# Performance work log

Measured on AMD Instinct MI355X. Metric: run time of the kernel, lower is better.

## Reference

```python
import jax, jax.numpy as jnp
import numpy as np

B, C = 8, 256
GRID = 128          # H = W = grid_size
N = GRID * GRID     # 16384 tokens
WS = 8              # swin window size
NH = 8              # num heads
DH = C // NH        # head dim = 32
HID = int(C * 4.0)  # mlp hidden = 1024
EPS = 1e-5


def _ln(x, g, b):
    m = jnp.mean(x, axis=-1, keepdims=True)
    v = jnp.mean(jnp.square(x - m), axis=-1, keepdims=True)
    return (x - m) * jax.lax.rsqrt(v + EPS) * g + b


def setup_inputs() -> dict:
    key = jax.random.key(0)
    ks = jax.random.split(key, 6)
    s = 0.02
    return {
        "x": jax.random.normal(ks[0], (B, N, C), jnp.float32),
        "ln1_g": jnp.ones((C,), jnp.float32), "ln1_b": jnp.zeros((C,), jnp.float32),
        "in_w": jax.random.normal(ks[1], (3 * C, C), jnp.float32) * s,
        "in_b": jnp.zeros((3 * C,), jnp.float32),
        "out_w": jax.random.normal(ks[2], (C, C), jnp.float32) * s,
        "out_b": jnp.zeros((C,), jnp.float32),
        "ln2_g": jnp.ones((C,), jnp.float32), "ln2_b": jnp.zeros((C,), jnp.float32),
        "w1": jax.random.normal(ks[3], (HID, C), jnp.float32) * s,
        "b1": jnp.zeros((HID,), jnp.float32),
        "w2": jax.random.normal(ks[4], (C, HID), jnp.float32) * s,
        "b2": jnp.zeros((C,), jnp.float32),
    }


def reference(x, ln1_g, ln1_b, in_w, in_b, out_w, out_b, ln2_g, ln2_b, w1, b1, w2, b2):
    shortcut = x
    xn = _ln(x, ln1_g, ln1_b)
    # window partition: [B,N,C] -> [B,H,W,C] -> [B*nW, WS*WS, C]
    xw = (xn.reshape(B, GRID // WS, WS, GRID // WS, WS, C)
            .transpose(0, 1, 3, 2, 4, 5)
            .reshape(-1, WS * WS, C))
    # torch nn.MultiheadAttention: fused in-proj, scale 1/sqrt(head_dim)
    qkv = xw @ in_w.T + in_b                      # [nW, T, 3C]
    q, k, v = jnp.split(qkv, 3, axis=-1)
    def heads(t):
        return t.reshape(t.shape[0], t.shape[1], NH, DH).transpose(0, 2, 1, 3)
    q, k, v = heads(q), heads(k), heads(v)        # [nW, NH, T, DH]
    scores = jnp.einsum('whtd,whsd->whts', q, k) * (1.0 / np.sqrt(DH))
    att = jax.nn.softmax(scores, axis=-1)
    o = jnp.einsum('whts,whsd->whtd', att, v)     # [nW, NH, T, DH]
    o = o.transpose(0, 2, 1, 3).reshape(-1, WS * WS, C)
    o = o @ out_w.T + out_b
    # window reverse: [B*nW, WS, WS, C] -> [B, N, C]
    x_attn = (o.reshape(B, GRID // WS, GRID // WS, WS, WS, C)
                .transpose(0, 1, 3, 2, 4, 5)
                .reshape(B, N, C))
    x = shortcut + x_attn
    h = _ln(x, ln2_g, ln2_b)
    h = jax.nn.gelu(h @ w1.T + b1, approximate=False)  # torch nn.GELU = exact erf
    return x + h @ w2.T + b2
```

## Files before the change

### kernel.cpp

```cpp
#include <hip/hip_runtime.h>
#include <hip/hip_bf16.h>
#include <cstdint>

#define DEVINL __device__ __forceinline__

using bf16 = __hip_bfloat16;
typedef __bf16 bf16x8 __attribute__((ext_vector_type(8)));
typedef float f32x4 __attribute__((ext_vector_type(4)));
typedef unsigned short u16x8 __attribute__((ext_vector_type(8)));

static constexpr int MTOK = 131072;

DEVINL void async_ld16(const void* g, void* l) {
  __builtin_amdgcn_global_load_lds(
      (__attribute__((address_space(1))) void*)(g),
      (__attribute__((address_space(3))) void*)(l), 16, 0, 0);
}

DEVINL unsigned short bfbits(float v) {
  bf16 h = __float2bfloat16(v);
  return *reinterpret_cast<unsigned short*>(&h);
}

DEVINL long pkaddr(long m, int k, int KP) {
  const long tile = m >> 7;
  const int row = (int)(m & 127);
  const int panel = k >> 6;
  const int c8 = ((k & 63) >> 3) ^ (row & 7);
  return ((tile * KP + panel) * 1024 + row * 8 + c8) * 8 + (k & 7);
}

__global__ __launch_bounds__(256) void cvt_w2(
    const float* __restrict__ ow, const float* __restrict__ w1,
    const float* __restrict__ w2, bf16* __restrict__ out) {
  int i = blockIdx.x * 256 + threadIdx.x;
  float v; long base; int n, k, KP;
  if (i < 65536)        { v = ow[i]; base = 0;      n = i >> 8;  k = i & 255;  KP = 4; }
  else if (i < 327680)  { int j = i - 65536;  v = w1[j]; base = 65536;  n = j >> 8;  k = j & 255;  KP = 4; }
  else                  { int j = i - 327680; v = w2[j]; base = 327680; n = j >> 10; k = j & 1023; KP = 16; }
  out[base + pkaddr(n, k, KP)] = __float2bfloat16(v);
}

template <bool REMAP>
__global__ __launch_bounds__(256) void ln_kern(
    const float* __restrict__ x, const float* __restrict__ gw,
    const float* __restrict__ bw, bf16* __restrict__ out) {
  const int lane = threadIdx.x & 63;
  const int wv = threadIdx.x >> 6;
  const long tok = (long)blockIdx.x * 4 + wv;
  const float4 v = *(const float4*)(x + tok * 256 + lane * 4);
  float s = v.x + v.y + v.z + v.w;
#pragma unroll
  for (int off = 32; off > 0; off >>= 1) s += __shfl_xor(s, off);
  const float mean = s * (1.0f / 256.0f);
  const float dx = v.x - mean, dy = v.y - mean, dz = v.z - mean, dw = v.w - mean;
  float q = dx * dx + dy * dy + dz * dz + dw * dw;
#pragma unroll
  for (int off = 32; off > 0; off >>= 1) q += __shfl_xor(q, off);
  const float inv = rsqrtf(q * (1.0f / 256.0f) + 1e-5f);
  long m;
  if (REMAP) {
    const int b = (int)(tok >> 14);
    const int n = (int)(tok & 16383);
    const int row = n >> 7, col = n & 127;
    const int w = b * 256 + (row >> 3) * 16 + (col >> 3);
    const int t = (row & 7) * 8 + (col & 7);
    m = (long)w * 64 + t;
  } else {
    m = tok;
  }
  const float4 g = *(const float4*)(gw + lane * 4);
  const float4 bb = *(const float4*)(bw + lane * 4);
  ushort4 o;
  o.x = bfbits(dx * inv * g.x + bb.x);
  o.y = bfbits(dy * inv * g.y + bb.y);
  o.z = bfbits(dz * inv * g.z + bb.z);
  o.w = bfbits(dw * inv * g.w + bb.w);
  *(ushort4*)((unsigned short*)out + pkaddr(m, lane * 4, 4)) = o;
}

enum { EPI_QKV = 0, EPI_OUTPROJ = 1, EPI_GELU = 2, EPI_RESID = 3 };

template <int KP, int EPI, bool BF32>
__global__ __launch_bounds__(256) void gemm_db(
    const bf16* __restrict__ A, const void* __restrict__ Bw,
    const float* __restrict__ bias,
    bf16* __restrict__ oQ, bf16* __restrict__ oK, bf16* __restrict__ oV,
    const float* __restrict__ resid, float* __restrict__ of32,
    bf16* __restrict__ obf) {
  __shared__ __align__(16) unsigned short smem[32768];
  const int tid = threadIdx.x;
  const int lane = tid & 63, wv = tid >> 6;
  const int quad = lane >> 4, l16 = lane & 15;
  const int wm = wv >> 1, wn = wv & 1;
  const int gx = gridDim.x;
  const int nwg = gx * gridDim.y;
  const int orig = blockIdx.x + gx * blockIdx.y;
  const int wg = (orig & 7) * (nwg >> 3) + (orig >> 3);
  const int ntile = wg % gx;
  const long mtile = wg / gx;
  const long m0 = mtile * 128;
  const int n0 = ntile * 128;

  const bf16* Bp = (const bf16*)Bw;
  const float* Bf = (const float*)Bw;
  float4 br[4][2];

  auto stageA = [&](int i, int buf) {
    const bf16* Apan = A + (mtile * KP + i) * 8192;
#pragma unroll
    for (int p = 0; p < 4; ++p) {
      const int f = p * 256 + tid;
      async_ld16(Apan + f * 8, (char*)smem + buf * 16384 + f * 16);
    }
  };
  auto stageB = [&](int i, int buf) {
    const bf16* Bpan = Bp + ((long)ntile * KP + i) * 8192;
#pragma unroll
    for (int p = 0; p < 4; ++p) {
      const int f = p * 256 + tid;
      async_ld16(Bpan + f * 8, (char*)smem + 32768 + buf * 16384 + f * 16);
    }
  };
  auto issueB = [&](int i) {
#pragma unroll
    for (int p = 0; p < 4; ++p) {
      const int f = p * 256 + tid, row = f >> 3;
      const int chunk = (f & 7) ^ (row & 7);
      const float* src = Bf + (long)(n0 + row) * 256 + i * 64 + chunk * 8;
      br[p][0] = *(const float4*)(src);
      br[p][1] = *(const float4*)(src + 4);
    }
  };
  auto writeB = [&](int buf) {
#pragma unroll
    for (int p = 0; p < 4; ++p) {
      const int f = p * 256 + tid;
      u16x8 o;
      o[0] = bfbits(br[p][0].x); o[1] = bfbits(br[p][0].y);
      o[2] = bfbits(br[p][0].z); o[3] = bfbits(br[p][0].w);
      o[4] = bfbits(br[p][1].x); o[5] = bfbits(br[p][1].y);
      o[6] = bfbits(br[p][1].z); o[7] = bfbits(br[p][1].w);
      *(u16x8*)((char*)smem + 32768 + buf * 16384 + f * 16) = o;
    }
  };

  const f32x4 fz = {0.f, 0.f, 0.f, 0.f};
  f32x4 acc[4][4];
#pragma unroll
  for (int a = 0; a < 4; ++a) {
#pragma unroll
    for (int b = 0; b < 4; ++b) acc[a][b] = fz;
  }

  if constexpr (BF32) { issueB(0); stageA(0, 0); }
  else                { stageA(0, 0); stageB(0, 0); }

#pragma unroll 1
  for (int i = 0; i < KP; ++i) {
    if constexpr (BF32) writeB(i & 1);
    __syncthreads();
    if (i + 1 < KP) {
      if constexpr (BF32) { issueB(i + 1); stageA(i + 1, (i + 1) & 1); }
      else                { stageA(i + 1, (i + 1) & 1); stageB(i + 1, (i + 1) & 1); }
    }
    const unsigned short* Asb = smem + (i & 1) * 8192;
    const unsigned short* Bsb = smem + 16384 + (i & 1) * 8192;
#pragma unroll
    for (int kk = 0; kk < 2; ++kk) {
      bf16x8 af[4], bfr[4];
#pragma unroll
      for (int mt = 0; mt < 4; ++mt) {
        const int row = wm * 64 + mt * 16 + l16;
        const int c8 = (kk * 4 + quad) ^ (row & 7);
        af[mt] = *(const bf16x8*)(Asb + row * 64 + c8 * 8);
      }
#pragma unroll
      for (int nt = 0; nt < 4; ++nt) {
        const int row = wn * 64 + nt * 16 + l16;
        const int c8 = (kk * 4 + quad) ^ (row & 7);
        bfr[nt] = *(const bf16x8*)(Bsb + row * 64 + c8 * 8);
      }
#pragma unroll
      for (int mt = 0; mt < 4; ++mt) {
#pragma unroll
        for (int nt = 0; nt < 4; ++nt) {
          acc[mt][nt] = __builtin_amdgcn_mfma_f32_16x16x32_bf16(
              af[mt], bfr[nt], acc[mt][nt], 0, 0, 0);
        }
      }
    }
  }

  if constexpr (EPI == EPI_QKV) {
    const int region = n0 >> 8;
    float bj4[4];
#pragma unroll
    for (int nt = 0; nt < 4; ++nt) bj4[nt] = bias[n0 + wn * 64 + nt * 16 + l16];
    __syncthreads();
    if (region < 2) {
#pragma unroll
      for (int mt = 0; mt < 4; ++mt) {
#pragma unroll
        for (int nt = 0; nt < 4; ++nt) {
          const int j_l = wn * 64 + nt * 16 + l16;
#pragma unroll
          for (int r = 0; r < 4; ++r) {
            const int m_l = wm * 64 + mt * 16 + quad * 4 + r;
            smem[m_l * 136 + j_l] = bfbits(acc[mt][nt][r] + bj4[nt]);
          }
        }
      }
    } else {
#pragma unroll
      for (int mt = 0; mt < 4; ++mt) {
#pragma unroll
        for (int nt = 0; nt < 4; ++nt) {
          const int j_l = wn * 64 + nt * 16 + l16;
          const int m_b = wm * 64 + mt * 16 + quad * 4;
          ushort4 pk;
          pk.x = bfbits(acc[mt][nt][0] + bj4[nt]);
          pk.y = bfbits(acc[mt][nt][1] + bj4[nt]);
          pk.z = bfbits(acc[mt][nt][2] + bj4[nt]);
          pk.w = bfbits(acc[mt][nt][3] + bj4[nt]);
          *(ushort4*)(smem + j_l * 136 + m_b) = pk;
        }
      }
    }
    __syncthreads();
    bf16* dst0 = (region == 0) ? oQ : ((region == 1) ? oK : oV);
    const int hbase = (n0 >> 5) & 7;
    const long w0 = m0 >> 6;
    if (region < 2) {
#pragma unroll
      for (int p = 0; p < 8; ++p) {
        const int u = p * 256 + tid;
        const int c = u >> 8, rr = u & 255;
        const int t = rr >> 2, d0 = (rr & 3) * 8;
        const unsigned short* src = smem + ((c >> 2) * 64 + t) * 136 + (c & 3) * 32 + d0;
        const long hb = (w0 + (c >> 2)) * 8 + hbase + (c & 3);
        *(u16x8*)((unsigned short*)dst0 + (hb * 64 + t) * 32 + d0) = *(const u16x8*)src;
      }
    } else {
#pragma unroll
      for (int p = 0; p < 8; ++p) {
        const int u = p * 256 + tid;
        const int c = u >> 8, rr = u & 255;
        const int d = rr >> 3, t0 = (rr & 7) * 8;
        const unsigned short* src = smem + ((c & 3) * 32 + d) * 136 + (c >> 2) * 64 + t0;
        const long hb = (w0 + (c >> 2)) * 8 + hbase + (c & 3);
        *(u16x8*)((unsigned short*)dst0 + (hb * 32 + d) * 64 + t0) = *(const u16x8*)src;
      }
    }
  } else {
#pragma unroll
    for (int mt = 0; mt < 4; ++mt) {
#pragma unroll
      for (int nt = 0; nt < 4; ++nt) {
        const long mb = m0 + wm * 64 + mt * 16 + quad * 4;
        const int j = n0 + wn * 64 + nt * 16 + l16;
        const float bj = bias[j];
#pragma unroll
        for (int r = 0; r < 4; ++r) {
          const long m = mb + r;
          const float v = acc[mt][nt][r] + bj;
          if constexpr (EPI == EPI_OUTPROJ) {
            const int w = (int)(m >> 6), t = (int)(m & 63);
            const int b = w >> 8, wi = w & 255;
            const int row = (wi >> 4) * 8 + (t >> 3);
            const int col = (wi & 15) * 8 + (t & 7);
            const long addr = ((long)b * 16384 + row * 128 + col) * 256 + j;
            of32[addr] = v + resid[addr];
          } else {
            const long addr = m * 256 + j;
            of32[addr] += v;
          }
        }
      }
    }
  }
}

__global__ __launch_bounds__(256, 1) void mlp_fused(
    const bf16* __restrict__ A, const bf16* __restrict__ W1p,
    const bf16* __restrict__ W2p, const float* __restrict__ b1,
    const float* __restrict__ b2, float* __restrict__ out) {
  __shared__ __align__(16) unsigned short smem[65536];
  unsigned short* Ares = smem;
  unsigned short* Wbuf = smem + 32768;
  unsigned short* Pbuf = smem + 49152;
  const int tid = threadIdx.x;
  const int lane = tid & 63;
  const int wv = tid >> 6;
  const int quad = lane >> 4, l16 = lane & 15;
  const int wm = wv >> 1, wn = wv & 1;
  const long mtile = blockIdx.x;

  auto stageW = [&](const bf16* wp, int buf) {
#pragma unroll
    for (int c = 0; c < 4; ++c) {
      const int f = c * 256 + tid;
      async_ld16(wp + f * 8, (char*)(Wbuf + buf * 8192) + f * 16);
    }
  };
  auto wptr = [&](int u) -> const bf16* {
    const int hcu = u >> 3, su = u & 7;
    return (su < 4) ? W1p + (hcu * 4 + su) * 8192
                    : W2p + ((((su >= 6) ? 16 : 0) + hcu * 2 + (su & 1))) * 8192;
  };
  auto mm = [&](const unsigned short* Abase, const unsigned short* Bbase,
                int arow0, int brow0, f32x4 (&acc)[4][4]) {
#pragma unroll
    for (int kk = 0; kk < 2; ++kk) {
      bf16x8 af[4], bfr[4];
#pragma unroll
      for (int x = 0; x < 4; ++x) {
        const int row = arow0 + x * 16 + l16;
        const int c8 = (kk * 4 + quad) ^ (row & 7);
        af[x] = *(const bf16x8*)(Abase + row * 64 + c8 * 8);
      }
#pragma unroll
      for (int x = 0; x < 4; ++x) {
        const int row = brow0 + x * 16 + l16;
        const int c8 = (kk * 4 + quad) ^ (row & 7);
        bfr[x] = *(const bf16x8*)(Bbase + row * 64 + c8 * 8);
      }
#pragma unroll
      for (int a = 0; a < 4; ++a) {
#pragma unroll
        for (int b = 0; b < 4; ++b) {
          acc[a][b] = __builtin_amdgcn_mfma_f32_16x16x32_bf16(
              af[a], bfr[b], acc[a][b], 0, 0, 0);
        }
      }
    }
  };

  {
    const bf16* Ap = A + mtile * 32768;
#pragma unroll
    for (int c = 0; c < 16; ++c) {
      const int f = c * 256 + tid;
      async_ld16(Ap + f * 8, (char*)Ares + f * 16);
    }
    stageW(W1p, 0);
  }

  const f32x4 fz = {0.f, 0.f, 0.f, 0.f};
  f32x4 acc2a[4][4], acc2b[4][4];
#pragma unroll
  for (int a = 0; a < 4; ++a) {
#pragma unroll
    for (int b = 0; b < 4; ++b) { acc2a[a][b] = fz; acc2b[a][b] = fz; }
  }

#pragma unroll 1
  for (int hc = 0; hc < 8; ++hc) {
    f32x4 acc1[4][4];
#pragma unroll
    for (int a = 0; a < 4; ++a) {
#pragma unroll
      for (int b = 0; b < 4; ++b) acc1[a][b] = fz;
    }
    f32x4 b1v[4];
#pragma unroll
    for (int s = 0; s < 4; ++s) {
      const int t = hc * 8 + s;
      __syncthreads();
      stageW(wptr(t + 1), (t + 1) & 1);
      if (s == 2) {
#pragma unroll
        for (int x = 0; x < 4; ++x)
          b1v[x] = *(const f32x4*)(b1 + hc * 128 + wn * 64 + x * 16 + quad * 4);
      }
      mm(Wbuf + (t & 1) * 8192, Ares + s * 8192, wn * 64, wm * 64, acc1);
    }
#pragma unroll
    for (int ht = 0; ht < 4; ++ht) {
#pragma unroll
      for (int mt = 0; mt < 4; ++mt) {
        const int m_l = wm * 64 + mt * 16 + l16;
        ushort4 pk;
#pragma unroll
        for (int r = 0; r < 4; ++r) {
          const float v = acc1[ht][mt][r] + b1v[ht][r];
          const float g = 0.5f * v * (1.0f + erff(v * 0.70710678118654752f));
          ((unsigned short*)&pk)[r] = bfbits(g);
        }
        const int c8p = (ht * 2 + (quad >> 1)) ^ (m_l & 7);
        *(ushort4*)(Pbuf + wn * 8192 + m_l * 64 + c8p * 8 + (quad & 1) * 4) = pk;
      }
    }
    {
      const int t = hc * 8 + 4;
      __syncthreads();
      stageW(wptr(t + 1), (t + 1) & 1);
      mm(Pbuf, Wbuf + (t & 1) * 8192, wm * 64, wn * 64, acc2a);
    }
    {
      const int t = hc * 8 + 5;
      __syncthreads();
      stageW(wptr(t + 1), (t + 1) & 1);
      mm(Pbuf + 8192, Wbuf + (t & 1) * 8192, wm * 64, wn * 64, acc2a);
    }
    {
      const int t = hc * 8 + 6;
      __syncthreads();
      stageW(wptr(t + 1), (t + 1) & 1);
      mm(Pbuf, Wbuf + (t & 1) * 8192, wm * 64, wn * 64, acc2b);
    }
    {
      const int t = hc * 8 + 7;
      __syncthreads();
      if (t + 1 < 64) stageW(wptr(t + 1), (t + 1) & 1);
      mm(Pbuf + 8192, Wbuf + (t & 1) * 8192, wm * 64, wn * 64, acc2b);
    }
  }

  const long m0 = mtile * 128;
  float b2a[4], b2b[4];
#pragma unroll
  for (int nt = 0; nt < 4; ++nt) {
    b2a[nt] = b2[wn * 64 + nt * 16 + l16];
    b2b[nt] = b2[128 + wn * 64 + nt * 16 + l16];
  }
#pragma unroll
  for (int mt = 0; mt < 4; ++mt) {
#pragma unroll
    for (int nt = 0; nt < 4; ++nt) {
      const long mb = m0 + wm * 64 + mt * 16 + quad * 4;
      const int ja = wn * 64 + nt * 16 + l16;
#pragma unroll
      for (int r = 0; r < 4; ++r) {
        out[(mb + r) * 256 + ja] += acc2a[mt][nt][r] + b2a[nt];
        out[(mb + r) * 256 + ja + 128] += acc2b[mt][nt][r] + b2b[nt];
      }
    }
  }
}

__global__ __launch_bounds__(256) void attn_kern(
    const bf16* __restrict__ Qb, const bf16* __restrict__ Kb,
    const bf16* __restrict__ Vtb, bf16* __restrict__ O) {
  __shared__ __align__(16) unsigned short P[4][64 * 72];
  __shared__ __align__(16) unsigned short Cw[4][64 * 72];
  const int lane = threadIdx.x & 63;
  const int wv = threadIdx.x >> 6;
  const int quad = lane >> 4, l16 = lane & 15;
  const long w = blockIdx.x;
  unsigned short* Pw = &P[wv][0];
  unsigned short* Cww = &Cw[wv][0];
  const float SC = 0.17677669529663689f;
  const f32x4 fz = {0.f, 0.f, 0.f, 0.f};

#pragma unroll 1
  for (int hi = 0; hi < 2; ++hi) {
    const int h = wv * 2 + hi;
    const bf16* qp = Qb + ((w * 8 + h) * 64) * 32;
    const bf16* kp = Kb + ((w * 8 + h) * 64) * 32;
    const bf16* vt = Vtb + ((w * 8 + h) * 32) * 64;

    bf16x8 qf[4], kf[4];
#pragma unroll
    for (int mt = 0; mt < 4; ++mt)
      qf[mt] = *(const bf16x8*)(qp + (mt * 16 + l16) * 32 + quad * 8);
#pragma unroll
    for (int nt = 0; nt < 4; ++nt)
      kf[nt] = *(const bf16x8*)(kp + (nt * 16 + l16) * 32 + quad * 8);

    f32x4 s[4][4];
#pragma unroll
    for (int a = 0; a < 4; ++a) {
#pragma unroll
      for (int b = 0; b < 4; ++b) s[a][b] = fz;
    }
#pragma unroll
    for (int mt = 0; mt < 4; ++mt) {
#pragma unroll
      for (int nt = 0; nt < 4; ++nt) {
        s[mt][nt] = __builtin_amdgcn_mfma_f32_16x16x32_bf16(qf[mt], kf[nt],
                                                            s[mt][nt], 0, 0, 0);
      }
    }

#pragma unroll
    for (int mt = 0; mt < 4; ++mt) {
#pragma unroll
      for (int r = 0; r < 4; ++r) {
        float a0 = s[mt][0][r] * SC, a1 = s[mt][1][r] * SC;
        float a2 = s[mt][2][r] * SC, a3 = s[mt][3][r] * SC;
        float mx = fmaxf(fmaxf(a0, a1), fmaxf(a2, a3));
#pragma unroll
        for (int off = 8; off > 0; off >>= 1) mx = fmaxf(mx, __shfl_xor(mx, off));
        a0 = __expf(a0 - mx); a1 = __expf(a1 - mx);
        a2 = __expf(a2 - mx); a3 = __expf(a3 - mx);
        float sm = a0 + a1 + a2 + a3;
#pragma unroll
        for (int off = 8; off > 0; off >>= 1) sm += __shfl_xor(sm, off);
        const float iv = 1.0f / sm;
        const int rp = (mt * 16 + quad * 4 + r) * 72;
        Pw[rp + l16]      = bfbits(a0 * iv);
        Pw[rp + 16 + l16] = bfbits(a1 * iv);
        Pw[rp + 32 + l16] = bfbits(a2 * iv);
        Pw[rp + 48 + l16] = bfbits(a3 * iv);
      }
    }

    bf16x8 vf[2][2];
#pragma unroll
    for (int kt = 0; kt < 2; ++kt) {
#pragma unroll
      for (int dt = 0; dt < 2; ++dt)
        vf[kt][dt] = *(const bf16x8*)(vt + (dt * 16 + l16) * 64 + kt * 32 + quad * 8);
    }
    f32x4 oa[4][2];
#pragma unroll
    for (int a = 0; a < 4; ++a) { oa[a][0] = fz; oa[a][1] = fz; }
#pragma unroll
    for (int mt = 0; mt < 4; ++mt) {
      const unsigned short* pr = Pw + (mt * 16 + l16) * 72 + quad * 8;
      const bf16x8 p0 = *(const bf16x8*)(pr);
      const bf16x8 p1 = *(const bf16x8*)(pr + 32);
#pragma unroll
      for (int dt = 0; dt < 2; ++dt) {
        oa[mt][dt] = __builtin_amdgcn_mfma_f32_16x16x32_bf16(p0, vf[0][dt], oa[mt][dt], 0, 0, 0);
        oa[mt][dt] = __builtin_amdgcn_mfma_f32_16x16x32_bf16(p1, vf[1][dt], oa[mt][dt], 0, 0, 0);
      }
    }

#pragma unroll
    for (int mt = 0; mt < 4; ++mt) {
#pragma unroll
      for (int dt = 0; dt < 2; ++dt) {
#pragma unroll
        for (int r = 0; r < 4; ++r) {
          const int m_l = mt * 16 + quad * 4 + r;
          const int j_l = hi * 32 + dt * 16 + l16;
          Cww[m_l * 72 + j_l] = bfbits(oa[mt][dt][r]);
        }
      }
    }
  }

  __syncthreads();
  const long tile = w >> 1;
  const int half = (int)(w & 1);
#pragma unroll
  for (int p = 0; p < 8; ++p) {
    const int u = p * 64 + lane;
    const int row = u >> 3, c8 = u & 7;
    const unsigned short* src = Cww + row * 72 + ((c8 ^ (row & 7)) * 8);
    unsigned short* dst = (unsigned short*)O +
        ((tile * 4 + wv) * 1024 + (half * 64 + row) * 8 + c8) * 8;
    *(u16x8*)dst = *(const u16x8*)src;
  }
}

extern "C" void kernel_launch(void* const* d_in, const int* in_sizes, int n_in,
                              void* d_out, int out_size, void* d_ws, size_t ws_size,
                              hipStream_t stream) {
  const float* x     = (const float*)d_in[0];
  const float* ln1g  = (const float*)d_in[1];
  const float* ln1b  = (const float*)d_in[2];
  const float* in_w  = (const float*)d_in[3];
  const float* in_b  = (const float*)d_in[4];
  const float* out_w = (const float*)d_in[5];
  const float* out_b = (const float*)d_in[6];
  const float* ln2g  = (const float*)d_in[7];
  const float* ln2b  = (const float*)d_in[8];
  const float* w1    = (const float*)d_in[9];
  const float* b1    = (const float*)d_in[10];
  const float* w2    = (const float*)d_in[11];
  const float* b2    = (const float*)d_in[12];
  float* out = (float*)d_out;

  char* ws = (char*)d_ws;
  const size_t MB = 1ull << 20;
  bf16* XW   = (bf16*)ws;
  bf16* Qb   = (bf16*)(ws + 64 * MB);
  bf16* Kb   = (bf16*)(ws + 128 * MB);
  bf16* Vtb  = (bf16*)(ws + 192 * MB);
  bf16* WB   = (bf16*)(ws + 64 * MB);
  bf16* Wo   = WB;
  bf16* W1c  = WB + 65536;
  bf16* W2c  = WB + 327680;
  bf16* Obuf = XW;
  bf16* Hbuf = XW;

  ln_kern<true><<<MTOK / 4, 256, 0, stream>>>(x, ln1g, ln1b, XW);
  gemm_db<4, EPI_QKV, true><<<dim3(6, MTOK / 128), 256, 0, stream>>>(
      XW, in_w, in_b, Qb, Kb, Vtb, nullptr, nullptr, nullptr);
  attn_kern<<<2048, 256, 0, stream>>>(Qb, Kb, Vtb, Obuf);
  cvt_w2<<<2304, 256, 0, stream>>>(out_w, w1, w2, WB);
  gemm_db<4, EPI_OUTPROJ, false><<<dim3(2, MTOK / 128), 256, 0, stream>>>(
      Obuf, Wo, out_b, nullptr, nullptr, nullptr, x, out, nullptr);
  ln_kern<false><<<MTOK / 4, 256, 0, stream>>>(out, ln2g, ln2b, Hbuf);
  mlp_fused<<<MTOK / 128, 256, 0, stream>>>(Hbuf, W1c, W2c, b1, b2, out);
}
```

Baseline: 822.1 us.

## Shrink fused MLP row tile to 64 and stream A to allow two blocks per CU

```diff
diff --git a/kernel.cpp b/kernel.cpp
--- a/kernel.cpp
+++ b/kernel.cpp
@@ -79,15 +79,14 @@
   *(ushort4*)((unsigned short*)out + pkaddr(m, lane * 4, 4)) = o;
 }
 
-enum { EPI_QKV = 0, EPI_OUTPROJ = 1, EPI_GELU = 2, EPI_RESID = 3 };
+enum { EPI_QKV = 0, EPI_OUTPROJ = 1 };
 
 template <int KP, int EPI, bool BF32>
 __global__ __launch_bounds__(256) void gemm_db(
     const bf16* __restrict__ A, const void* __restrict__ Bw,
     const float* __restrict__ bias,
     bf16* __restrict__ oQ, bf16* __restrict__ oK, bf16* __restrict__ oV,
-    const float* __restrict__ resid, float* __restrict__ of32,
-    bf16* __restrict__ obf) {
+    const float* __restrict__ resid, float* __restrict__ of32) {
   __shared__ __align__(16) unsigned short smem[32768];
   const int tid = threadIdx.x;
   const int lane = tid & 63, wv = tid >> 6;
@@ -264,122 +263,122 @@
         for (int r = 0; r < 4; ++r) {
           const long m = mb + r;
           const float v = acc[mt][nt][r] + bj;
-          if constexpr (EPI == EPI_OUTPROJ) {
-            const int w = (int)(m >> 6), t = (int)(m & 63);
-            const int b = w >> 8, wi = w & 255;
-            const int row = (wi >> 4) * 8 + (t >> 3);
-            const int col = (wi & 15) * 8 + (t & 7);
-            const long addr = ((long)b * 16384 + row * 128 + col) * 256 + j;
-            of32[addr] = v + resid[addr];
-          } else {
-            const long addr = m * 256 + j;
-            of32[addr] += v;
-          }
-        }
-      }
-    }
-  }
-}
-
-__global__ __launch_bounds__(256, 1) void mlp_fused(
+          const int w = (int)(m >> 6), t = (int)(m & 63);
+          const int b = w >> 8, wi = w & 255;
+          const int row = (wi >> 4) * 8 + (t >> 3);
+          const int col = (wi & 15) * 8 + (t & 7);
+          const long addr = ((long)b * 16384 + row * 128 + col) * 256 + j;
+          of32[addr] = v + resid[addr];
+        }
+      }
+    }
+  }
+}
+
+__global__ __launch_bounds__(256, 2) void mlp_fused(
     const bf16* __restrict__ A, const bf16* __restrict__ W1p,
     const bf16* __restrict__ W2p, const float* __restrict__ b1,
     const float* __restrict__ b2, float* __restrict__ out) {
-  __shared__ __align__(16) unsigned short smem[65536];
-  unsigned short* Ares = smem;
-  unsigned short* Wbuf = smem + 32768;
-  unsigned short* Pbuf = smem + 49152;
+  __shared__ __align__(16) unsigned short smem[40960];
+  unsigned short* Pbuf = smem + 32768;
   const int tid = threadIdx.x;
   const int lane = tid & 63;
   const int wv = tid >> 6;
   const int quad = lane >> 4, l16 = lane & 15;
-  const int wm = wv >> 1, wn = wv & 1;
-  const long mtile = blockIdx.x;
-
-  auto stageW = [&](const bf16* wp, int buf) {
-#pragma unroll
-    for (int c = 0; c < 4; ++c) {
-      const int f = c * 256 + tid;
-      async_ld16(wp + f * 8, (char*)(Wbuf + buf * 8192) + f * 16);
+  const int bm = blockIdx.x;
+  const bf16* Ab = A + (long)(bm >> 1) * 32768 + (bm & 1) * 4096;
+
+  auto stage = [&](int g) {
+    char* dst = (char*)smem + (g & 1) * 32768;
+    const int hc = g / 6, t = g - hc * 6;
+    if (t < 4) {
+      const bf16* wp = W1p + (hc * 4 + t) * 8192;
+#pragma unroll
+      for (int c = 0; c < 4; ++c) {
+        const int f = c * 256 + tid;
+        async_ld16(wp + f * 8, dst + f * 16);
+      }
+      const bf16* ap = Ab + t * 8192;
+#pragma unroll
+      for (int c = 0; c < 2; ++c) {
+        const int f = c * 256 + tid;
+        async_ld16(ap + f * 8, dst + 16384 + f * 16);
+      }
+    } else {
+#pragma unroll
+      for (int rt = 0; rt < 2; ++rt) {
+        const bf16* wp = W2p + (rt * 16 + hc * 2 + (t - 4)) * 8192;
+#pragma unroll
+        for (int c = 0; c < 4; ++c) {
+          const int f = c * 256 + tid;
+          async_ld16(wp + f * 8, dst + rt * 16384 + f * 16);
+        }
+      }
     }
   };
-  auto wptr = [&](int u) -> const bf16* {
-    const int hcu = u >> 3, su = u & 7;
-    return (su < 4) ? W1p + (hcu * 4 + su) * 8192
-                    : W2p + ((((su >= 6) ? 16 : 0) + hcu * 2 + (su & 1))) * 8192;
-  };
-  auto mm = [&](const unsigned short* Abase, const unsigned short* Bbase,
-                int arow0, int brow0, f32x4 (&acc)[4][4]) {
-#pragma unroll
-    for (int kk = 0; kk < 2; ++kk) {
-      bf16x8 af[4], bfr[4];
-#pragma unroll
-      for (int x = 0; x < 4; ++x) {
-        const int row = arow0 + x * 16 + l16;
-        const int c8 = (kk * 4 + quad) ^ (row & 7);
-        af[x] = *(const bf16x8*)(Abase + row * 64 + c8 * 8);
-      }
-#pragma unroll
-      for (int x = 0; x < 4; ++x) {
-        const int row = brow0 + x * 16 + l16;
-        const int c8 = (kk * 4 + quad) ^ (row & 7);
-        bfr[x] = *(const bf16x8*)(Bbase + row * 64 + c8 * 8);
-      }
-#pragma unroll
-      for (int a = 0; a < 4; ++a) {
-#pragma unroll
-        for (int b = 0; b < 4; ++b) {
-          acc[a][b] = __builtin_amdgcn_mfma_f32_16x16x32_bf16(
-              af[a], bfr[b], acc[a][b], 0, 0, 0);
-        }
-      }
-    }
-  };
-
-  {
-    const bf16* Ap = A + mtile * 32768;
-#pragma unroll
-    for (int c = 0; c < 16; ++c) {
-      const int f = c * 256 + tid;
-      async_ld16(Ap + f * 8, (char*)Ares + f * 16);
-    }
-    stageW(W1p, 0);
-  }
 
   const f32x4 fz = {0.f, 0.f, 0.f, 0.f};
-  f32x4 acc2a[4][4], acc2b[4][4];
+  f32x4 acc2[4][4];
 #pragma unroll
   for (int a = 0; a < 4; ++a) {
 #pragma unroll
-    for (int b = 0; b < 4; ++b) { acc2a[a][b] = fz; acc2b[a][b] = fz; }
-  }
+    for (int b = 0; b < 4; ++b) acc2[a][b] = fz;
+  }
+
+  stage(0);
 
 #pragma unroll 1
   for (int hc = 0; hc < 8; ++hc) {
-    f32x4 acc1[4][4];
-#pragma unroll
-    for (int a = 0; a < 4; ++a) {
+    f32x4 acc1[2][4];
+#pragma unroll
+    for (int a = 0; a < 2; ++a) {
 #pragma unroll
       for (int b = 0; b < 4; ++b) acc1[a][b] = fz;
     }
-    f32x4 b1v[4];
+    f32x4 b1v[2];
+#pragma unroll
+    for (int ht = 0; ht < 2; ++ht)
+      b1v[ht] = *(const f32x4*)(b1 + hc * 128 + wv * 32 + ht * 16 + quad * 4);
+
 #pragma unroll
     for (int s = 0; s < 4; ++s) {
-      const int t = hc * 8 + s;
+      const int g = hc * 6 + s;
       __syncthreads();
-      stageW(wptr(t + 1), (t + 1) & 1);
-      if (s == 2) {
-#pragma unroll
-        for (int x = 0; x < 4; ++x)
-          b1v[x] = *(const f32x4*)(b1 + hc * 128 + wn * 64 + x * 16 + quad * 4);
-      }
-      mm(Wbuf + (t & 1) * 8192, Ares + s * 8192, wn * 64, wm * 64, acc1);
-    }
-#pragma unroll
-    for (int ht = 0; ht < 4; ++ht) {
+      stage(g + 1);
+      const unsigned short* buf = smem + (g & 1) * 16384;
+#pragma unroll
+      for (int kk = 0; kk < 2; ++kk) {
+        bf16x8 af[2], bfr[4];
+#pragma unroll
+        for (int x = 0; x < 2; ++x) {
+          const int row = wv * 32 + x * 16 + l16;
+          const int c8 = (kk * 4 + quad) ^ (row & 7);
+          af[x] = *(const bf16x8*)(buf + row * 64 + c8 * 8);
+        }
+#pragma unroll
+        for (int x = 0; x < 4; ++x) {
+          const int row = x * 16 + l16;
+          const int c8 = (kk * 4 + quad) ^ (row & 7);
+          bfr[x] = *(const bf16x8*)(buf + 8192 + row * 64 + c8 * 8);
+        }
+#pragma unroll
+        for (int a = 0; a < 2; ++a) {
+#pragma unroll
+          for (int b = 0; b < 4; ++b) {
+            acc1[a][b] = __builtin_amdgcn_mfma_f32_16x16x32_bf16(
+                af[a], bfr[b], acc1[a][b], 0, 0, 0);
+          }
+        }
+      }
+    }
+
+#pragma unroll
+    for (int ht = 0; ht < 2; ++ht) {
+      const int k0 = wv * 32 + ht * 16 + quad * 4;
+      const int panel = k0 >> 6, kin = k0 & 63;
 #pragma unroll
       for (int mt = 0; mt < 4; ++mt) {
-        const int m_l = wm * 64 + mt * 16 + l16;
+        const int m = mt * 16 + l16;
         ushort4 pk;
 #pragma unroll
         for (int r = 0; r < 4; ++r) {
@@ -387,53 +386,58 @@
           const float g = 0.5f * v * (1.0f + erff(v * 0.70710678118654752f));
           ((unsigned short*)&pk)[r] = bfbits(g);
         }
-        const int c8p = (ht * 2 + (quad >> 1)) ^ (m_l & 7);
-        *(ushort4*)(Pbuf + wn * 8192 + m_l * 64 + c8p * 8 + (quad & 1) * 4) = pk;
-      }
-    }
-    {
-      const int t = hc * 8 + 4;
+        const int c8 = (kin >> 3) ^ (m & 7);
+        *(ushort4*)(Pbuf + panel * 4096 + m * 64 + c8 * 8 + (kin & 7)) = pk;
+      }
+    }
+
+#pragma unroll
+    for (int kp = 0; kp < 2; ++kp) {
+      const int g = hc * 6 + 4 + kp;
       __syncthreads();
-      stageW(wptr(t + 1), (t + 1) & 1);
-      mm(Pbuf, Wbuf + (t & 1) * 8192, wm * 64, wn * 64, acc2a);
-    }
-    {
-      const int t = hc * 8 + 5;
-      __syncthreads();
-      stageW(wptr(t + 1), (t + 1) & 1);
-      mm(Pbuf + 8192, Wbuf + (t & 1) * 8192, wm * 64, wn * 64, acc2a);
-    }
-    {
-      const int t = hc * 8 + 6;
-      __syncthreads();
-      stageW(wptr(t + 1), (t + 1) & 1);
-      mm(Pbuf, Wbuf + (t & 1) * 8192, wm * 64, wn * 64, acc2b);
-    }
-    {
-      const int t = hc * 8 + 7;
-      __syncthreads();
-      if (t + 1 < 64) stageW(wptr(t + 1), (t + 1) & 1);
-      mm(Pbuf + 8192, Wbuf + (t & 1) * 8192, wm * 64, wn * 64, acc2b);
-    }
-  }
-
-  const long m0 = mtile * 128;
-  float b2a[4], b2b[4];
-#pragma unroll
-  for (int nt = 0; nt < 4; ++nt) {
-    b2a[nt] = b2[wn * 64 + nt * 16 + l16];
-    b2b[nt] = b2[128 + wn * 64 + nt * 16 + l16];
-  }
+      if (g + 1 < 48) stage(g + 1);
+      const unsigned short* buf = smem + (g & 1) * 16384;
+      const unsigned short* pp = Pbuf + kp * 4096;
+#pragma unroll
+      for (int kk = 0; kk < 2; ++kk) {
+        bf16x8 af[4], bfr[4];
+#pragma unroll
+        for (int x = 0; x < 4; ++x) {
+          const int row = x * 16 + l16;
+          const int c8 = (kk * 4 + quad) ^ (row & 7);
+          af[x] = *(const bf16x8*)(pp + row * 64 + c8 * 8);
+        }
+#pragma unroll
+        for (int x = 0; x < 4; ++x) {
+          const int row = (wv & 1) * 64 + x * 16 + l16;
+          const int c8 = (kk * 4 + quad) ^ (row & 7);
+          bfr[x] = *(const bf16x8*)(buf + (wv >> 1) * 8192 + row * 64 + c8 * 8);
+        }
+#pragma unroll
+        for (int a = 0; a < 4; ++a) {
+#pragma unroll
+          for (int b = 0; b < 4; ++b) {
+            acc2[a][b] = __builtin_amdgcn_mfma_f32_16x16x32_bf16(
+                af[a], bfr[b], acc2[a][b], 0, 0, 0);
+          }
+        }
+      }
+    }
+  }
+
+  const long m0 = (long)bm * 64;
+  float b2v[4];
+#pragma unroll
+  for (int nt = 0; nt < 4; ++nt) b2v[nt] = b2[wv * 64 + nt * 16 + l16];
 #pragma unroll
   for (int mt = 0; mt < 4; ++mt) {
 #pragma unroll
     for (int nt = 0; nt < 4; ++nt) {
-      const long mb = m0 + wm * 64 + mt * 16 + quad * 4;
-      const int ja = wn * 64 + nt * 16 + l16;
+      const int n = wv * 64 + nt * 16 + l16;
 #pragma unroll
       for (int r = 0; r < 4; ++r) {
-        out[(mb + r) * 256 + ja] += acc2a[mt][nt][r] + b2a[nt];
-        out[(mb + r) * 256 + ja + 128] += acc2b[mt][nt][r] + b2b[nt];
+        const long m = m0 + mt * 16 + quad * 4 + r;
+        out[m * 256 + n] += acc2[mt][nt][r] + b2v[nt];
       }
     }
   }
@@ -589,11 +593,11 @@
 
   ln_kern<true><<<MTOK / 4, 256, 0, stream>>>(x, ln1g, ln1b, XW);
   gemm_db<4, EPI_QKV, true><<<dim3(6, MTOK / 128), 256, 0, stream>>>(
-      XW, in_w, in_b, Qb, Kb, Vtb, nullptr, nullptr, nullptr);
+      XW, in_w, in_b, Qb, Kb, Vtb, nullptr, nullptr);
   attn_kern<<<2048, 256, 0, stream>>>(Qb, Kb, Vtb, Obuf);
   cvt_w2<<<2304, 256, 0, stream>>>(out_w, w1, w2, WB);
   gemm_db<4, EPI_OUTPROJ, false><<<dim3(2, MTOK / 128), 256, 0, stream>>>(
-      Obuf, Wo, out_b, nullptr, nullptr, nullptr, x, out, nullptr);
+      Obuf, Wo, out_b, nullptr, nullptr, nullptr, x, out);
   ln_kern<false><<<MTOK / 4, 256, 0, stream>>>(out, ln2g, ln2b, Hbuf);
-  mlp_fused<<<MTOK / 128, 256, 0, stream>>>(Hbuf, W1c, W2c, b1, b2, out);
-}
+  mlp_fused<<<MTOK / 64, 256, 0, stream>>>(Hbuf, W1c, W2c, b1, b2, out);
+}
```

New measurement: 763.0 us. 1.08x faster.
